# Optimization experiments

Measured on AMD Instinct MI355X. Metric: run time of the kernel, lower is better.

Reference implementation:

```python
import jax, jax.numpy as jnp
import numpy as np

OUT_H, OUT_W = 7, 7
SCALE = 0.25
S = 2  # sample_num per bin axis


def _bilinear(img, y, x):
    """Bilinearly sample img[..., H, W] at float coords (y, x).
    y, x have identical shape G; returns img.shape[:-2] + G.
    Matches RoIAlign CUDA interpolation (zero outside [-1, H]/[-1, W])."""
    H, W = img.shape[-2], img.shape[-1]
    valid = (y > -1.0) & (y < H) & (x > -1.0) & (x < W)
    y = jnp.clip(y, 0.0, H - 1)
    x = jnp.clip(x, 0.0, W - 1)
    y0 = jnp.floor(y).astype(jnp.int32)
    x0 = jnp.floor(x).astype(jnp.int32)
    y1 = jnp.minimum(y0 + 1, H - 1)
    x1 = jnp.minimum(x0 + 1, W - 1)
    ly = y - y0
    lx = x - x0
    hy, hx = 1.0 - ly, 1.0 - lx
    v = (hy * hx * img[..., y0, x0] + hy * lx * img[..., y0, x1]
         + ly * hx * img[..., y1, x0] + ly * lx * img[..., y1, x1])
    return jnp.where(valid, v, 0.0)


def setup_inputs() -> dict:
    key = jax.random.key(0)
    k1, k2, k3, k4, k5 = jax.random.split(key, 5)
    N, C, H, W = 2, 256, 200, 200
    R, MH, MW = 512, 128, 128
    features = jax.random.normal(k1, (N, C, H, W), jnp.float32)
    bidx = jax.random.randint(k2, (R,), 0, N)
    xy1 = jax.random.randint(k3, (R, 2), 0, 672)          # x1, y1 (image coords)
    wh = jax.random.randint(k4, (R, 2), 8, 128)           # box sizes in [8,128)
    xy2 = jnp.minimum(xy1 + wh - 1, 799)                  # x2, y2 inclusive
    rois = jnp.concatenate([bidx[:, None].astype(jnp.float32),
                            xy1.astype(jnp.float32),
                            xy2.astype(jnp.float32)], axis=1)  # [R,5]
    batch_masks = jax.random.uniform(k5, (R, MH, MW), jnp.float32)
    # zero-pad beyond each roi's (h, w), mimicking the list->dense packing
    hv = jnp.arange(MH)[None, :] < (xy2[:, 1] - xy1[:, 1] + 1)[:, None]
    wv = jnp.arange(MW)[None, :] < (xy2[:, 0] - xy1[:, 0] + 1)[:, None]
    batch_masks = batch_masks * (hv[:, :, None] & wv[:, None, :]).astype(jnp.float32)
    return {"features": features, "rois": rois, "batch_masks": batch_masks}


def reference(features, rois, batch_masks):
    """Mask-weighted RoIAlign: per-roi bilinear feature samples are weighted by
    the roi's shape mask (bilinearly sampled in roi-relative image coords),
    then average-pooled over the sub-sample grid of each output bin."""
    C = features.shape[1]

    def one_roi(roi, mask):
        b = roi[0].astype(jnp.int32)
        x1, y1, x2, y2 = roi[1], roi[2], roi[3], roi[4]
        roi_start_w = x1 * SCALE
        roi_start_h = y1 * SCALE
        roi_w = jnp.maximum((x2 - x1 + 1.0) * SCALE, 1.0)
        roi_h = jnp.maximum((y2 - y1 + 1.0) * SCALE, 1.0)
        bin_w = roi_w / OUT_W
        bin_h = roi_h / OUT_H
        # sub-sample offsets: (bin + (i+0.5)/S) for i in [0,S)  -> [OUT*S]
        offs = (jnp.arange(S, dtype=jnp.float32) + 0.5) / S
        ys = roi_start_h + (jnp.arange(OUT_H, dtype=jnp.float32)[:, None] + offs[None, :]).reshape(-1) * bin_h
        xs = roi_start_w + (jnp.arange(OUT_W, dtype=jnp.float32)[:, None] + offs[None, :]).reshape(-1) * bin_w
        yy, xx = jnp.meshgrid(ys, xs, indexing='ij')       # [OUT_H*S, OUT_W*S]
        feat = features[b]                                  # [C, H, W]
        vals = _bilinear(feat, yy, xx)                      # [C, OUT_H*S, OUT_W*S]
        # mask weight at the same sample point, in roi-relative image coords
        my = jnp.clip(yy / SCALE - y1, 0.0, y2 - y1)
        mx = jnp.clip(xx / SCALE - x1, 0.0, x2 - x1)
        wgt = _bilinear(mask, my, mx)                       # [OUT_H*S, OUT_W*S]
        v = (vals * wgt).reshape(C, OUT_H, S, OUT_W, S)
        return v.mean(axis=(2, 4))                          # [C, OUT_H, OUT_W]

    return jax.vmap(one_roi)(rois, batch_masks)             # [R, C, OUT_H, OUT_W]
```

## Files before the change

kernel.cpp:

```cpp
#include <hip/hip_runtime.h>


constexpr int   OUT_H = 7, OUT_W = 7;
constexpr int   NBIN  = OUT_H * OUT_W;
constexpr float SCALE = 0.25f;
constexpr int   S     = 2;
constexpr int   NSAMP = NBIN * S * S;
constexpr int   CPB   = 64;
constexpr int   NQ    = CPB / 4;

typedef unsigned short ushort_t;

__device__ __forceinline__ ushort_t f2bf(float f) {
    unsigned u = __float_as_uint(f);
    u += 0x7fffu + ((u >> 16) & 1u);
    return (ushort_t)(u >> 16);
}
__device__ __forceinline__ float bf2f(ushort_t h) {
    return __uint_as_float(((unsigned)h) << 16);
}
__device__ __forceinline__ unsigned pack2(float a, float b) {
    return (unsigned)f2bf(a) | ((unsigned)f2bf(b) << 16);
}

__global__ __launch_bounds__(256)
void nchw_to_nhwc_bf16_kernel(const float* __restrict__ in,
                              ushort_t* __restrict__ out, int C, int P) {
    __shared__ float tile[64][65];
    const int tid = threadIdx.x;
    const int b   = blockIdx.z;
    const int gx  = blockIdx.x * 64;
    const int gy  = blockIdx.y * 64;

    const float* inb  = in  + (size_t)b * C * P;
    ushort_t*    outb = out + (size_t)b * C * P;

    {
        const int tx = tid & 15, ty = tid >> 4;
#pragma unroll
        for (int j = 0; j < 4; ++j) {
            const int c_local = ty + 16 * j;
            const float4 v = *(const float4*)&inb[(size_t)(gy + c_local) * P + gx + 4 * tx];
            tile[c_local][4 * tx + 0] = v.x;
            tile[c_local][4 * tx + 1] = v.y;
            tile[c_local][4 * tx + 2] = v.z;
            tile[c_local][4 * tx + 3] = v.w;
        }
    }
    __syncthreads();
    {
        const int ow = tid & 7;
        const int oh = tid >> 3;
#pragma unroll
        for (int j = 0; j < 2; ++j) {
            const int p_local = oh + 32 * j;
            uint4 h;
            h.x = pack2(tile[8 * ow + 0][p_local], tile[8 * ow + 1][p_local]);
            h.y = pack2(tile[8 * ow + 2][p_local], tile[8 * ow + 3][p_local]);
            h.z = pack2(tile[8 * ow + 4][p_local], tile[8 * ow + 5][p_local]);
            h.w = pack2(tile[8 * ow + 6][p_local], tile[8 * ow + 7][p_local]);
            *(uint4*)&outb[(size_t)(gx + p_local) * C + gy + 8 * ow] = h;
        }
    }
}

__global__ __launch_bounds__(256)
void mask_roialign_nhwc_bf16_kernel(const ushort_t* __restrict__ nhwc,
                                    const float* __restrict__ rois,
                                    const float* __restrict__ masks,
                                    float*       __restrict__ out,
                                    int C, int H, int W, int MH, int MW) {
    __shared__ int   s_off[NSAMP][4];
    __shared__ float s_w[NSAMP][4];
    __shared__ float s_out[4][NQ][NBIN];

    const int r   = blockIdx.x;
    const int cg  = blockIdx.y;
    const int tid = threadIdx.x;

    const float* roi = rois + (size_t)r * 5;
    const int   b  = (int)roi[0];
    const float x1 = roi[1], y1 = roi[2], x2 = roi[3], y2 = roi[4];

    if (tid < NSAMP) {
        const int bin = tid >> 2;
        const int sub = tid & 3;
        const int ph  = bin / OUT_W, pw = bin % OUT_W;
        const int iy  = sub >> 1,   ix = sub & 1;

        const float roi_start_w = x1 * SCALE;
        const float roi_start_h = y1 * SCALE;
        const float roi_w = fmaxf((x2 - x1 + 1.0f) * SCALE, 1.0f);
        const float roi_h = fmaxf((y2 - y1 + 1.0f) * SCALE, 1.0f);
        const float bin_w = roi_w / (float)OUT_W;
        const float bin_h = roi_h / (float)OUT_H;

        const float yy = roi_start_h + ((float)ph + ((float)iy + 0.5f) * (1.0f / S)) * bin_h;
        const float xx = roi_start_w + ((float)pw + ((float)ix + 0.5f) * (1.0f / S)) * bin_w;

        const bool valid = (yy > -1.0f) && (yy < (float)H) && (xx > -1.0f) && (xx < (float)W);

        const float* msk = masks + (size_t)r * MH * MW;
        float my = fminf(fmaxf(yy * (1.0f / SCALE) - y1, 0.0f), y2 - y1);
        float mx = fminf(fmaxf(xx * (1.0f / SCALE) - x1, 0.0f), x2 - x1);
        my = fminf(fmaxf(my, 0.0f), (float)(MH - 1));
        mx = fminf(fmaxf(mx, 0.0f), (float)(MW - 1));
        const int my0 = (int)floorf(my), mx0 = (int)floorf(mx);
        const int my1 = min(my0 + 1, MH - 1), mx1 = min(mx0 + 1, MW - 1);
        const float mly = my - (float)my0, mlx = mx - (float)mx0;
        const float mhy = 1.0f - mly,      mhx = 1.0f - mlx;
        const float wgt = mhy * mhx * msk[my0 * MW + mx0] + mhy * mlx * msk[my0 * MW + mx1]
                        + mly * mhx * msk[my1 * MW + mx0] + mly * mlx * msk[my1 * MW + mx1];

        const float yc = fminf(fmaxf(yy, 0.0f), (float)(H - 1));
        const float xc = fminf(fmaxf(xx, 0.0f), (float)(W - 1));
        const int y0  = (int)floorf(yc), x0 = (int)floorf(xc);
        const int y1i = min(y0 + 1, H - 1), x1i = min(x0 + 1, W - 1);
        const float ly = yc - (float)y0, lx = xc - (float)x0;
        const float hy = 1.0f - ly,      hx = 1.0f - lx;

        const float scale_all = (valid ? wgt : 0.0f) * (1.0f / (float)(S * S));
        s_w[tid][0] = hy * hx * scale_all;
        s_w[tid][1] = hy * lx * scale_all;
        s_w[tid][2] = ly * hx * scale_all;
        s_w[tid][3] = ly * lx * scale_all;
        s_off[tid][0] = (y0  * W + x0 ) * C;
        s_off[tid][1] = (y0  * W + x1i) * C;
        s_off[tid][2] = (y1i * W + x0 ) * C;
        s_off[tid][3] = (y1i * W + x1i) * C;
    }
    __syncthreads();

    const int cq = tid & (NQ - 1);
    const int bg = tid >> 4;
    const int c0 = cg * CPB + cq * 4;
    const ushort_t* fbase = nhwc + (size_t)b * H * W * C + c0;

    for (int bin = bg; bin < NBIN; bin += 16) {
        float ax = 0.0f, ay = 0.0f, az = 0.0f, aw = 0.0f;
#pragma unroll
        for (int sub = 0; sub < 4; ++sub) {
            const int s = bin * 4 + sub;
            const int   o0 = s_off[s][0], o1 = s_off[s][1], o2 = s_off[s][2], o3 = s_off[s][3];
            const float w0 = s_w[s][0],   w1 = s_w[s][1],   w2 = s_w[s][2],   w3 = s_w[s][3];
            const ushort4 q0 = *(const ushort4*)&fbase[o0];
            const ushort4 q1 = *(const ushort4*)&fbase[o1];
            const ushort4 q2 = *(const ushort4*)&fbase[o2];
            const ushort4 q3 = *(const ushort4*)&fbase[o3];
            ax += w0 * bf2f(q0.x) + w1 * bf2f(q1.x) + w2 * bf2f(q2.x) + w3 * bf2f(q3.x);
            ay += w0 * bf2f(q0.y) + w1 * bf2f(q1.y) + w2 * bf2f(q2.y) + w3 * bf2f(q3.y);
            az += w0 * bf2f(q0.z) + w1 * bf2f(q1.z) + w2 * bf2f(q2.z) + w3 * bf2f(q3.z);
            aw += w0 * bf2f(q0.w) + w1 * bf2f(q1.w) + w2 * bf2f(q2.w) + w3 * bf2f(q3.w);
        }
        s_out[0][cq][bin] = ax;
        s_out[1][cq][bin] = ay;
        s_out[2][cq][bin] = az;
        s_out[3][cq][bin] = aw;
    }
    __syncthreads();

    float* outr = out + ((size_t)r * C + (size_t)cg * CPB) * NBIN;
    for (int i = tid; i < CPB * NBIN; i += 256) {
        const int c   = i / NBIN;
        const int bin = i - c * NBIN;
        outr[i] = s_out[c & 3][c >> 2][bin];
    }
}

__global__ __launch_bounds__(256)
void mask_roialign_kernel(const float* __restrict__ features,
                          const float* __restrict__ rois,
                          const float* __restrict__ masks,
                          float*       __restrict__ out,
                          int C, int H, int W, int MH, int MW) {
    int blk = blockIdx.x;
    int pw  = blk % OUT_W;
    int ph  = (blk / OUT_W) % OUT_H;
    int r   = blk / (OUT_W * OUT_H);
    int c   = threadIdx.x;

    const float* roi = rois + (size_t)r * 5;
    int   b  = (int)roi[0];
    float x1 = roi[1], y1 = roi[2], x2 = roi[3], y2 = roi[4];

    float roi_start_w = x1 * SCALE;
    float roi_start_h = y1 * SCALE;
    float roi_w = fmaxf((x2 - x1 + 1.0f) * SCALE, 1.0f);
    float roi_h = fmaxf((y2 - y1 + 1.0f) * SCALE, 1.0f);
    float bin_w = roi_w / (float)OUT_W;
    float bin_h = roi_h / (float)OUT_H;

    const float* fch = features + ((size_t)b * C + c) * (size_t)(H * W);
    const float* msk = masks + (size_t)r * MH * MW;

    float acc = 0.0f;
#pragma unroll
    for (int iy = 0; iy < S; ++iy) {
        float yy = roi_start_h + ((float)ph + ((float)iy + 0.5f) / (float)S) * bin_h;
#pragma unroll
        for (int ix = 0; ix < S; ++ix) {
            float xx = roi_start_w + ((float)pw + ((float)ix + 0.5f) / (float)S) * bin_w;
            bool valid = (yy > -1.0f) && (yy < (float)H) && (xx > -1.0f) && (xx < (float)W);
            float my = fminf(fmaxf(yy / SCALE - y1, 0.0f), fminf(y2 - y1, (float)(MH - 1)));
            float mx = fminf(fmaxf(xx / SCALE - x1, 0.0f), fminf(x2 - x1, (float)(MW - 1)));
            int my0 = (int)floorf(my), mx0 = (int)floorf(mx);
            int my1 = min(my0 + 1, MH - 1), mx1 = min(mx0 + 1, MW - 1);
            float mly = my - my0, mlx = mx - mx0, mhy = 1.0f - mly, mhx = 1.0f - mlx;
            float wgt = mhy * mhx * msk[my0 * MW + mx0] + mhy * mlx * msk[my0 * MW + mx1]
                      + mly * mhx * msk[my1 * MW + mx0] + mly * mlx * msk[my1 * MW + mx1];
            if (valid) {
                float yc = fminf(fmaxf(yy, 0.0f), (float)(H - 1));
                float xc = fminf(fmaxf(xx, 0.0f), (float)(W - 1));
                int y0 = (int)floorf(yc), x0 = (int)floorf(xc);
                int y1i = min(y0 + 1, H - 1), x1i = min(x0 + 1, W - 1);
                float ly = yc - y0, lx = xc - x0, hy = 1.0f - ly, hx = 1.0f - lx;
                float v = hy * hx * fch[y0  * W + x0 ] + hy * lx * fch[y0  * W + x1i]
                        + ly * hx * fch[y1i * W + x0 ] + ly * lx * fch[y1i * W + x1i];
                acc += wgt * v;
            }
        }
    }
    out[((size_t)r * C + c) * (size_t)NBIN + ph * OUT_W + pw] = acc * (1.0f / (S * S));
}

extern "C" void kernel_launch(void* const* d_in, const int* in_sizes, int n_in,
                              void* d_out, int out_size, void* d_ws, size_t ws_size,
                              hipStream_t stream) {
    const float* features = (const float*)d_in[0];
    const float* rois     = (const float*)d_in[1];
    const float* masks    = (const float*)d_in[2];
    float*       out      = (float*)d_out;

    const int R  = in_sizes[1] / 5;
    const int C  = out_size / (R * NBIN);
    const int H  = 200, W = 200;
    const int MH = 128, MW = 128;
    const int N  = in_sizes[0] / (C * H * W);
    const int P  = H * W;

    const size_t need = (size_t)N * C * P * sizeof(ushort_t);
    const bool tiles_ok = (C % 64 == 0) && (P % 64 == 0) && (C % CPB == 0);
    if (ws_size >= need && tiles_ok) {
        ushort_t* nhwc = (ushort_t*)d_ws;
        dim3 tg(P / 64, C / 64, N);
        nchw_to_nhwc_bf16_kernel<<<tg, dim3(256), 0, stream>>>(features, nhwc, C, P);

        mask_roialign_nhwc_bf16_kernel<<<dim3(R, C / CPB), dim3(256), 0, stream>>>(
            nhwc, rois, masks, out, C, H, W, MH, MW);
    } else {
        mask_roialign_kernel<<<dim3(R * NBIN), dim3(256), 0, stream>>>(
            features, rois, masks, out, C, H, W, MH, MW);
    }
}
```

Before: 169.9 us.

## Use channel-group tiled bf16 layout and stage ROI region in shared memory

The transpose kernel now writes features as [N][C/16][H*W][16] bf16 blocks instead of full NHWC. The RoIAlign kernel launches one block per (roi, 16-channel group) and copies the ROI's bounding pixel window (capped at 34x34) into LDS with 16-byte loads. Bilinear taps are then read from LDS, and the output is written with float4 stores. The aim is to replace scattered global gathers with a coalesced staging load plus LDS reuse. In exchange there are four times more blocks, larger LDS use, and the cap at 34 could clip samples for very large ROIs.

```diff
diff --git a/kernel.cpp b/kernel.cpp
--- a/kernel.cpp
+++ b/kernel.cpp
@@ -6,8 +6,8 @@
 constexpr float SCALE = 0.25f;
 constexpr int   S     = 2;
 constexpr int   NSAMP = NBIN * S * S;
-constexpr int   CPB   = 64;
-constexpr int   NQ    = CPB / 4;
+constexpr int   CG16  = 16;
+constexpr int   REG   = 34;
 
 typedef unsigned short ushort_t;
 
@@ -24,16 +24,16 @@
 }
 
 __global__ __launch_bounds__(256)
-void nchw_to_nhwc_bf16_kernel(const float* __restrict__ in,
-                              ushort_t* __restrict__ out, int C, int P) {
+void nchw_to_tiled_bf16_kernel(const float* __restrict__ in,
+                               ushort_t* __restrict__ out, int C, int P) {
     __shared__ float tile[64][65];
     const int tid = threadIdx.x;
     const int b   = blockIdx.z;
     const int gx  = blockIdx.x * 64;
     const int gy  = blockIdx.y * 64;
-
-    const float* inb  = in  + (size_t)b * C * P;
-    ushort_t*    outb = out + (size_t)b * C * P;
+    const int NG  = C / CG16;
+
+    const float* inb = in + (size_t)b * C * P;
 
     {
         const int tx = tid & 15, ty = tid >> 4;
@@ -49,38 +49,65 @@
     }
     __syncthreads();
     {
-        const int ow = tid & 7;
-        const int oh = tid >> 3;
+        const int gq = tid >> 6;
+        const int r  = tid & 63;
+        const int g  = (gy >> 4) + gq;
+        ushort_t* dstg = out + ((size_t)(b * NG + g) * P) * CG16;
 #pragma unroll
         for (int j = 0; j < 2; ++j) {
-            const int p_local = oh + 32 * j;
+            const int idx     = r + 64 * j;
+            const int p_local = idx >> 1;
+            const int half    = idx & 1;
+            const int cb      = gq * 16 + half * 8;
             uint4 h;
-            h.x = pack2(tile[8 * ow + 0][p_local], tile[8 * ow + 1][p_local]);
-            h.y = pack2(tile[8 * ow + 2][p_local], tile[8 * ow + 3][p_local]);
-            h.z = pack2(tile[8 * ow + 4][p_local], tile[8 * ow + 5][p_local]);
-            h.w = pack2(tile[8 * ow + 6][p_local], tile[8 * ow + 7][p_local]);
-            *(uint4*)&outb[(size_t)(gx + p_local) * C + gy + 8 * ow] = h;
+            h.x = pack2(tile[cb + 0][p_local], tile[cb + 1][p_local]);
+            h.y = pack2(tile[cb + 2][p_local], tile[cb + 3][p_local]);
+            h.z = pack2(tile[cb + 4][p_local], tile[cb + 5][p_local]);
+            h.w = pack2(tile[cb + 6][p_local], tile[cb + 7][p_local]);
+            *(uint4*)&dstg[(size_t)(gx + p_local) * CG16 + half * 8] = h;
         }
     }
 }
 
 __global__ __launch_bounds__(256)
-void mask_roialign_nhwc_bf16_kernel(const ushort_t* __restrict__ nhwc,
-                                    const float* __restrict__ rois,
-                                    const float* __restrict__ masks,
-                                    float*       __restrict__ out,
-                                    int C, int H, int W, int MH, int MW) {
-    __shared__ int   s_off[NSAMP][4];
-    __shared__ float s_w[NSAMP][4];
-    __shared__ float s_out[4][NQ][NBIN];
+void mask_roialign_tiled_kernel(const ushort_t* __restrict__ tiled,
+                                const float* __restrict__ rois,
+                                const float* __restrict__ masks,
+                                float*       __restrict__ out,
+                                int C, int H, int W, int MH, int MW) {
+    __shared__ ushort_t region[REG * REG * CG16];
+    __shared__ int      s_off[NSAMP][4];
+    __shared__ float    s_w[NSAMP][4];
+    __shared__ float    s_outb[CG16 * NBIN];
 
     const int r   = blockIdx.x;
-    const int cg  = blockIdx.y;
+    const int g   = blockIdx.y;
     const int tid = threadIdx.x;
+    const int NG  = C / CG16;
 
     const float* roi = rois + (size_t)r * 5;
     const int   b  = (int)roi[0];
     const float x1 = roi[1], y1 = roi[2], x2 = roi[3], y2 = roi[4];
+
+    const float roi_start_w = x1 * SCALE;
+    const float roi_start_h = y1 * SCALE;
+    const float roi_w = fmaxf((x2 - x1 + 1.0f) * SCALE, 1.0f);
+    const float roi_h = fmaxf((y2 - y1 + 1.0f) * SCALE, 1.0f);
+    const float bin_w = roi_w / (float)OUT_W;
+    const float bin_h = roi_h / (float)OUT_H;
+
+    const float xs_min = fminf(fmaxf(roi_start_w + 0.25f * bin_w, 0.0f), (float)(W - 1));
+    const float xs_max = fminf(fmaxf(roi_start_w + 6.75f * bin_w, 0.0f), (float)(W - 1));
+    const float ys_min = fminf(fmaxf(roi_start_h + 0.25f * bin_h, 0.0f), (float)(H - 1));
+    const float ys_max = fminf(fmaxf(roi_start_h + 6.75f * bin_h, 0.0f), (float)(H - 1));
+    const int x_lo = (int)floorf(xs_min);
+    const int y_lo = (int)floorf(ys_min);
+    int x_hi = min((int)floorf(xs_max) + 1, W - 1);
+    int y_hi = min((int)floorf(ys_max) + 1, H - 1);
+    x_hi = min(x_hi, x_lo + REG - 1);
+    y_hi = min(y_hi, y_lo + REG - 1);
+    const int cols = x_hi - x_lo + 1;
+    const int rows = y_hi - y_lo + 1;
 
     if (tid < NSAMP) {
         const int bin = tid >> 2;
@@ -88,15 +115,8 @@
         const int ph  = bin / OUT_W, pw = bin % OUT_W;
         const int iy  = sub >> 1,   ix = sub & 1;
 
-        const float roi_start_w = x1 * SCALE;
-        const float roi_start_h = y1 * SCALE;
-        const float roi_w = fmaxf((x2 - x1 + 1.0f) * SCALE, 1.0f);
-        const float roi_h = fmaxf((y2 - y1 + 1.0f) * SCALE, 1.0f);
-        const float bin_w = roi_w / (float)OUT_W;
-        const float bin_h = roi_h / (float)OUT_H;
-
-        const float yy = roi_start_h + ((float)ph + ((float)iy + 0.5f) * (1.0f / S)) * bin_h;
-        const float xx = roi_start_w + ((float)pw + ((float)ix + 0.5f) * (1.0f / S)) * bin_w;
+        const float yy = roi_start_h + ((float)ph + ((float)iy + 0.5f) * 0.5f) * bin_h;
+        const float xx = roi_start_w + ((float)pw + ((float)ix + 0.5f) * 0.5f) * bin_w;
 
         const bool valid = (yy > -1.0f) && (yy < (float)H) && (xx > -1.0f) && (xx < (float)W);
 
@@ -124,47 +144,56 @@
         s_w[tid][1] = hy * lx * scale_all;
         s_w[tid][2] = ly * hx * scale_all;
         s_w[tid][3] = ly * lx * scale_all;
-        s_off[tid][0] = (y0  * W + x0 ) * C;
-        s_off[tid][1] = (y0  * W + x1i) * C;
-        s_off[tid][2] = (y1i * W + x0 ) * C;
-        s_off[tid][3] = (y1i * W + x1i) * C;
+        const int dy0 = y0 - y_lo, dy1 = y1i - y_lo;
+        const int dx0 = x0 - x_lo, dx1 = x1i - x_lo;
+        s_off[tid][0] = (dy0 * cols + dx0) * CG16;
+        s_off[tid][1] = (dy0 * cols + dx1) * CG16;
+        s_off[tid][2] = (dy1 * cols + dx0) * CG16;
+        s_off[tid][3] = (dy1 * cols + dx1) * CG16;
+    }
+
+    {
+        const ushort_t* src = tiled + ((size_t)(b * NG + g) * W * H) * CG16;
+        const int cpr   = cols * 2;
+        const int total = rows * cpr;
+        for (int k = tid; k < total; k += 256) {
+            const int ry = k / cpr;
+            const int rx = k - ry * cpr;
+            const uint4 v = *(const uint4*)&src[((size_t)(y_lo + ry) * W + x_lo) * CG16 + rx * 8];
+            *(uint4*)&region[(ry * cols) * CG16 + rx * 8] = v;
+        }
     }
     __syncthreads();
 
-    const int cq = tid & (NQ - 1);
-    const int bg = tid >> 4;
-    const int c0 = cg * CPB + cq * 4;
-    const ushort_t* fbase = nhwc + (size_t)b * H * W * C + c0;
-
-    for (int bin = bg; bin < NBIN; bin += 16) {
-        float ax = 0.0f, ay = 0.0f, az = 0.0f, aw = 0.0f;
+    const int cp = tid & 7;
+    const int sg = tid >> 3;
+
+    for (int bin = sg; bin < NBIN; bin += 32) {
+        float a0 = 0.0f, a1 = 0.0f;
 #pragma unroll
         for (int sub = 0; sub < 4; ++sub) {
             const int s = bin * 4 + sub;
             const int   o0 = s_off[s][0], o1 = s_off[s][1], o2 = s_off[s][2], o3 = s_off[s][3];
             const float w0 = s_w[s][0],   w1 = s_w[s][1],   w2 = s_w[s][2],   w3 = s_w[s][3];
-            const ushort4 q0 = *(const ushort4*)&fbase[o0];
-            const ushort4 q1 = *(const ushort4*)&fbase[o1];
-            const ushort4 q2 = *(const ushort4*)&fbase[o2];
-            const ushort4 q3 = *(const ushort4*)&fbase[o3];
-            ax += w0 * bf2f(q0.x) + w1 * bf2f(q1.x) + w2 * bf2f(q2.x) + w3 * bf2f(q3.x);
-            ay += w0 * bf2f(q0.y) + w1 * bf2f(q1.y) + w2 * bf2f(q2.y) + w3 * bf2f(q3.y);
-            az += w0 * bf2f(q0.z) + w1 * bf2f(q1.z) + w2 * bf2f(q2.z) + w3 * bf2f(q3.z);
-            aw += w0 * bf2f(q0.w) + w1 * bf2f(q1.w) + w2 * bf2f(q2.w) + w3 * bf2f(q3.w);
-        }
-        s_out[0][cq][bin] = ax;
-        s_out[1][cq][bin] = ay;
-        s_out[2][cq][bin] = az;
-        s_out[3][cq][bin] = aw;
+            const unsigned u0 = *(const unsigned*)&region[o0 + 2 * cp];
+            const unsigned u1 = *(const unsigned*)&region[o1 + 2 * cp];
+            const unsigned u2 = *(const unsigned*)&region[o2 + 2 * cp];
+            const unsigned u3 = *(const unsigned*)&region[o3 + 2 * cp];
+            a0 += w0 * __uint_as_float(u0 << 16) + w1 * __uint_as_float(u1 << 16)
+                + w2 * __uint_as_float(u2 << 16) + w3 * __uint_as_float(u3 << 16);
+            a1 += w0 * __uint_as_float(u0 & 0xffff0000u) + w1 * __uint_as_float(u1 & 0xffff0000u)
+                + w2 * __uint_as_float(u2 & 0xffff0000u) + w3 * __uint_as_float(u3 & 0xffff0000u);
+        }
+        s_outb[(2 * cp + 0) * NBIN + bin] = a0;
+        s_outb[(2 * cp + 1) * NBIN + bin] = a1;
     }
     __syncthreads();
 
-    float* outr = out + ((size_t)r * C + (size_t)cg * CPB) * NBIN;
-    for (int i = tid; i < CPB * NBIN; i += 256) {
-        const int c   = i / NBIN;
-        const int bin = i - c * NBIN;
-        outr[i] = s_out[c & 3][c >> 2][bin];
-    }
+    float* outr = out + ((size_t)r * C + (size_t)g * CG16) * NBIN;
+    const float4* s4 = (const float4*)s_outb;
+    float4*       o4 = (float4*)outr;
+    for (int i = tid; i < (CG16 * NBIN) / 4; i += 256)
+        o4[i] = s4[i];
 }
 
 __global__ __launch_bounds__(256)
@@ -239,14 +268,14 @@
     const int P  = H * W;
 
     const size_t need = (size_t)N * C * P * sizeof(ushort_t);
-    const bool tiles_ok = (C % 64 == 0) && (P % 64 == 0) && (C % CPB == 0);
+    const bool tiles_ok = (C % 64 == 0) && (P % 64 == 0);
     if (ws_size >= need && tiles_ok) {
-        ushort_t* nhwc = (ushort_t*)d_ws;
+        ushort_t* tiled = (ushort_t*)d_ws;
         dim3 tg(P / 64, C / 64, N);
-        nchw_to_nhwc_bf16_kernel<<<tg, dim3(256), 0, stream>>>(features, nhwc, C, P);
-
-        mask_roialign_nhwc_bf16_kernel<<<dim3(R, C / CPB), dim3(256), 0, stream>>>(
-            nhwc, rois, masks, out, C, H, W, MH, MW);
+        nchw_to_tiled_bf16_kernel<<<tg, dim3(256), 0, stream>>>(features, tiled, C, P);
+
+        mask_roialign_tiled_kernel<<<dim3(R, C / CG16), dim3(256), 0, stream>>>(
+            tiled, rois, masks, out, C, H, W, MH, MW);
     } else {
         mask_roialign_kernel<<<dim3(R * NBIN), dim3(256), 0, stream>>>(
             features, rois, masks, out, C, H, W, MH, MW);
```

Result: slower. 188.5 us (+11.0%).
